# Kernel tuning notes

Measured on AMD Instinct MI355X. Metric: run time of the kernel, lower is better.

Reference implementation:

```python
import jax, jax.numpy as jnp
import numpy as np

N = 100000      # nodes
E = 1600000     # edges (avg degree 16)
D = 128         # in = hid = out dim


def setup_inputs() -> dict:
    key = jax.random.key(0)
    ks = jax.random.split(key, 7)
    x = jax.random.normal(ks[0], (N, D), dtype=jnp.float32)
    src = jax.random.randint(ks[1], (E,), 0, N, dtype=jnp.int32)
    dst = jax.random.randint(ks[2], (E,), 0, N, dtype=jnp.int32)
    s = 1.0 / np.sqrt(2 * D)  # torch Linear default init bound
    W0 = jax.random.uniform(ks[3], (D, 2 * D), jnp.float32, -s, s)
    b0 = jax.random.uniform(ks[4], (D,), jnp.float32, -s, s)
    W1 = jax.random.uniform(ks[5], (D, 2 * D), jnp.float32, -s, s)
    b1 = jax.random.uniform(ks[6], (D,), jnp.float32, -s, s)
    return {"x": x, "src": src, "dst": dst, "W0": W0, "b0": b0, "W1": W1, "b1": b1}


def graph_conv_left(x, src, dst):
    """DGL GraphConv(norm='left', weight=False, bias=False):
    h_v = sum_{(u->v) in E} x_u / max(outdeg(u), 1)."""
    n = x.shape[0]
    deg = jax.ops.segment_sum(jnp.ones_like(src, dtype=x.dtype), src, num_segments=n)
    deg = jnp.maximum(deg, 1.0)
    msgs = (x / deg[:, None])[src]          # [E, D] gather of normalized src feats
    return jax.ops.segment_sum(msgs, dst, num_segments=n)  # [N, D] scatter-add


def reference(x, src, dst, W0, b0, W1, b1):
    # layer 0: concat(self, agg) -> linear -> relu
    h = jnp.concatenate([x, graph_conv_left(x, src, dst)], axis=1)  # [N, 2D]
    h = jax.nn.relu(h @ W0.T + b0)                                  # [N, D]
    # layer 1 (output): concat -> linear (no relu)
    out = jnp.concatenate([h, graph_conv_left(h, src, dst)], axis=1) @ W1.T + b1
    return out
```

## Files before the change

### kernel.cpp

```cpp
#include <hip/hip_runtime.h>
#include <hip/hip_fp16.h>

#define DIM 128
#define CAP 64
#define BW_LOG 9
#define BW_NODES 512
#define MAXNB 256
#define SCAP 10240
#define CHUNK_P 2048
#define WSTRIDE 264

typedef _Float16 f16x8 __attribute__((ext_vector_type(8)));
typedef float f32x4 __attribute__((ext_vector_type(4)));
typedef unsigned int uint;

__global__ __launch_bounds__(256) void k_prep(const float* __restrict__ W0,
                                              const float* __restrict__ W1,
                                              const float* __restrict__ x,
                                              __half* __restrict__ Wh0,
                                              __half* __restrict__ Wh1,
                                              __half* __restrict__ fh,
                                              uint* __restrict__ curD,
                                              uint* __restrict__ curS,
                                              int NB, int nquadX) {
    int i = blockIdx.x * 256 + threadIdx.x;
    if (i < NB) { curD[i] = (uint)i * SCAP; curS[i] = (uint)i * SCAP; }
    const float* in; __half* out; int q;
    if (i < 8192)        { in = W0; out = Wh0; q = i; }
    else if (i < 16384)  { in = W1; out = Wh1; q = i - 8192; }
    else {
        q = i - 16384;
        if (q >= nquadX) return;
        in = x; out = fh;
    }
    float4 v = ((const float4*)in)[q];
    __half2* o = (__half2*)out;
    o[q * 2]     = __floats2half2_rn(v.x, v.y);
    o[q * 2 + 1] = __floats2half2_rn(v.z, v.w);
}

__global__ __launch_bounds__(256) void k_scatter(const int* __restrict__ src,
                                                 const int* __restrict__ dst,
                                                 uint* __restrict__ curD,
                                                 uint* __restrict__ curS,
                                                 uint* __restrict__ dbuf,
                                                 uint* __restrict__ sbuf,
                                                 int E, int NB, int nchunk) {
    __shared__ uint cb[MAXNB], bb[MAXNB], rb[MAXNB];
    for (int i = threadIdx.x; i < NB; i += 256) { cb[i] = 0; rb[i] = 0; }
    __syncthreads();
    bool isD = (int)blockIdx.x < nchunk;
    int chunk = isD ? blockIdx.x : blockIdx.x - nchunk;
    int e0 = chunk * CHUNK_P;
    int e1 = min(e0 + CHUNK_P, E);

    int4 sv[2], dv[2];
    bool ok[2];
    uint* cur  = isD ? curD : curS;
    uint* obuf = isD ? dbuf : sbuf;

#pragma unroll
    for (int q = 0; q < 2; ++q) {
        int i4 = (e0 >> 2) + q * 256 + (int)threadIdx.x;
        int e = i4 << 2;
        ok[q] = (e < e1);
        if (ok[q]) {
            sv[q] = ((const int4*)src)[i4];
            if (isD) dv[q] = ((const int4*)dst)[i4];
            int4 key = isD ? dv[q] : sv[q];
            atomicAdd(&cb[key.x >> BW_LOG], 1);
            atomicAdd(&cb[key.y >> BW_LOG], 1);
            atomicAdd(&cb[key.z >> BW_LOG], 1);
            atomicAdd(&cb[key.w >> BW_LOG], 1);
        }
    }
    __syncthreads();
    for (int i = threadIdx.x; i < NB; i += 256)
        if (cb[i]) bb[i] = atomicAdd(&cur[i], cb[i]);
    __syncthreads();
#pragma unroll
    for (int q = 0; q < 2; ++q) {
        if (!ok[q]) continue;
        int ks[4] = {isD ? dv[q].x : sv[q].x, isD ? dv[q].y : sv[q].y,
                     isD ? dv[q].z : sv[q].z, isD ? dv[q].w : sv[q].w};
        int ps[4] = {sv[q].x, sv[q].y, sv[q].z, sv[q].w};
#pragma unroll
        for (int k = 0; k < 4; ++k) {
            uint bkt = (uint)ks[k] >> BW_LOG;
            uint r = atomicAdd(&rb[bkt], 1);
            uint pos = bb[bkt] + r;
            uint pay = isD ? (((uint)(ks[k] & (BW_NODES - 1)) << 17) | (uint)ps[k])
                           : (uint)ps[k];
            if (pos < (bkt + 1) * SCAP) obuf[pos] = pay;
        }
    }
}

__global__ __launch_bounds__(256) void k_build_both(const uint* __restrict__ dbuf,
                                                    const uint* __restrict__ curD,
                                                    int* __restrict__ edge_pad,
                                                    int* __restrict__ cnt,
                                                    const uint* __restrict__ sbuf,
                                                    const uint* __restrict__ curS,
                                                    float* __restrict__ invd,
                                                    int N, int NB) {
    __shared__ uint cur[BW_NODES];
    for (int i = threadIdx.x; i < BW_NODES; i += 256) cur[i] = 0;
    __syncthreads();
    if ((int)blockIdx.x < NB) {
        int b = blockIdx.x;
        uint base = (uint)b * SCAP;
        uint total = curD[b] - base;
        if (total > SCAP) total = SCAP;
        int node0 = b << BW_LOG;
        for (uint i = threadIdx.x; i < total; i += 256) {
            uint v = dbuf[base + i];
            uint local = v >> 17;
            uint s = v & 0x1FFFFu;
            uint slot = atomicAdd(&cur[local], 1);
            if (slot < CAP)
                edge_pad[(size_t)(node0 + (int)local) * CAP + slot] = (int)s;
        }
        __syncthreads();
        for (int i = threadIdx.x; i < BW_NODES; i += 256) {
            int node = node0 + i;
            if (node < N) cnt[node] = (int)(cur[i] < CAP ? cur[i] : CAP);
        }
    } else {
        int b = blockIdx.x - NB;
        uint base = (uint)b * SCAP;
        uint total = curS[b] - base;
        if (total > SCAP) total = SCAP;
        int node0 = b << BW_LOG;
        for (uint i = threadIdx.x; i < total; i += 256)
            atomicAdd(&cur[sbuf[base + i] & (BW_NODES - 1)], 1);
        __syncthreads();
        for (int i = threadIdx.x; i < BW_NODES; i += 256) {
            int node = node0 + i;
            if (node < N) {
                uint d = cur[i];
                invd[node] = 1.0f / (float)(d > 1 ? d : 1);
            }
        }
    }
}

__global__ __launch_bounds__(256) void k_gather(const __half* __restrict__ feat,
                                                const float* __restrict__ invd,
                                                const int* __restrict__ edge_pad,
                                                const int* __restrict__ cnt_arr,
                                                __half* __restrict__ agg, int n) {
    int v = blockIdx.x * 4 + (threadIdx.x >> 6);
    int lane = threadIdx.x & 63;
    int quad = lane >> 4;
    int lq   = lane & 15;
    if (v >= n) return;
    int cnt = cnt_arr[v];
    if (cnt > CAP) cnt = CAP;

    int u_lane = 0;
    float w_lane = 0.f;
    if (lane < cnt) {
        u_lane = edge_pad[(size_t)v * CAP + lane];
        w_lane = invd[u_lane];
    }

    float acc[8] = {0.f, 0.f, 0.f, 0.f, 0.f, 0.f, 0.f, 0.f};
    int cntUp = (cnt + 7) & ~7;
    for (int j = 0; j < cntUp; j += 8) {
        int   ua = __shfl(u_lane, j + quad);
        float wa = __shfl(w_lane, j + quad);
        int   ub = __shfl(u_lane, j + 4 + quad);
        float wb = __shfl(w_lane, j + 4 + quad);
        uint4 ra = *(const uint4*)&feat[(size_t)ua * 128 + lq * 8];
        uint4 rb = *(const uint4*)&feat[(size_t)ub * 128 + lq * 8];
        const __half2* pa = (const __half2*)&ra;
        const __half2* pb = (const __half2*)&rb;
#pragma unroll
        for (int i = 0; i < 4; ++i) {
            float2 fa = __half22float2(pa[i]);
            float2 fb = __half22float2(pb[i]);
            acc[2 * i]     = fmaf(fa.x, wa, acc[2 * i]);
            acc[2 * i + 1] = fmaf(fa.y, wa, acc[2 * i + 1]);
            acc[2 * i]     = fmaf(fb.x, wb, acc[2 * i]);
            acc[2 * i + 1] = fmaf(fb.y, wb, acc[2 * i + 1]);
        }
    }
#pragma unroll
    for (int off = 16; off <= 32; off <<= 1) {
#pragma unroll
        for (int i = 0; i < 8; ++i) acc[i] += __shfl_xor(acc[i], off);
    }
    if (quad == 0) {
        __half2 o[4];
#pragma unroll
        for (int i = 0; i < 4; ++i) o[i] = __floats2half2_rn(acc[2 * i], acc[2 * i + 1]);
        *(uint4*)&agg[(size_t)v * 128 + lq * 8] = *(const uint4*)o;
    }
}

template <bool RELU, bool OUT16>
__global__ __launch_bounds__(256) void k_gemm_f16(const _Float16* __restrict__ A0,
                                                  const _Float16* __restrict__ A1,
                                                  const _Float16* __restrict__ Wh,
                                                  const float* __restrict__ bias,
                                                  float* __restrict__ out32,
                                                  _Float16* __restrict__ out16,
                                                  int n_rows) {
    __shared__ _Float16 Ws[128 * WSTRIDE];
    int tid  = threadIdx.x;
    int wave = tid >> 6;
    int lane = tid & 63;
    int quad = lane >> 4;
    int l16  = lane & 15;
    int m0 = blockIdx.x * 128 + wave * 32;

#pragma unroll
    for (int i = 0; i < 16; ++i) {
        int chunk = i * 256 + tid;
        int r = chunk >> 5;
        int c = (chunk & 31) * 8;
        *(f16x8*)&Ws[r * WSTRIDE + c] = *(const f16x8*)&Wh[r * 256 + c];
    }
    __syncthreads();

    f32x4 acc[2][8] = {};

    int ra = m0 + l16;
    int rb = m0 + 16 + l16;
    size_t r0 = (size_t)(ra < n_rows ? ra : 0);
    size_t r1 = (size_t)(rb < n_rows ? rb : 0);

#pragma unroll
    for (int ks = 0; ks < 8; ++ks) {
        int k0 = ks * 32;
        const _Float16* Ab = (k0 < 128) ? A0 : A1;
        int kk = (k0 & 127) + quad * 8;
        f16x8 a0 = *(const f16x8*)&Ab[r0 * 128 + kk];
        f16x8 a1 = *(const f16x8*)&Ab[r1 * 128 + kk];
        f16x8 b[8];
#pragma unroll
        for (int t = 0; t < 8; ++t)
            b[t] = *(const f16x8*)&Ws[(t * 16 + l16) * WSTRIDE + k0 + quad * 8];
#pragma unroll
        for (int t = 0; t < 8; ++t) {
            acc[0][t] = __builtin_amdgcn_mfma_f32_16x16x32_f16(a0, b[t], acc[0][t], 0, 0, 0);
            acc[1][t] = __builtin_amdgcn_mfma_f32_16x16x32_f16(a1, b[t], acc[1][t], 0, 0, 0);
        }
    }

#pragma unroll
    for (int t = 0; t < 8; ++t) {
        int col = t * 16 + l16;
        float bv = bias[col];
#pragma unroll
        for (int g = 0; g < 2; ++g) {
#pragma unroll
            for (int r = 0; r < 4; ++r) {
                int row = m0 + g * 16 + quad * 4 + r;
                if (row < n_rows) {
                    float v = acc[g][t][r] + bv;
                    if (RELU) v = fmaxf(v, 0.f);
                    if (OUT16) out16[(size_t)row * 128 + col] = (_Float16)v;
                    else       out32[(size_t)row * 128 + col] = v;
                }
            }
        }
    }
}

extern "C" void kernel_launch(void* const* d_in, const int* in_sizes, int n_in,
                              void* d_out, int out_size, void* d_ws, size_t ws_size,
                              hipStream_t stream) {
    const float* x  = (const float*)d_in[0];
    const int*   src = (const int*)d_in[1];
    const int*   dst = (const int*)d_in[2];
    const float* W0 = (const float*)d_in[3];
    const float* b0 = (const float*)d_in[4];
    const float* W1 = (const float*)d_in[5];
    const float* b1 = (const float*)d_in[6];
    int N = in_sizes[0] / DIM;
    int E = in_sizes[1];
    float* out = (float*)d_out;
    int NB = (N + BW_NODES - 1) >> BW_LOG;

    char* p = (char*)d_ws;
    uint* curD = (uint*)p; p += MAXNB * 4;
    uint* curS = (uint*)p; p += MAXNB * 4;
    int*   edge_pad = (int*)p;   p += (size_t)N * CAP * 4;
    int*   cnt      = (int*)p;   p += (size_t)N * 4;
    float* invd     = (float*)p; p += (size_t)N * 4;
    char*  uni = p;
    size_t bufSz = (size_t)2 * NB * SCAP * 4;
    size_t uniSz = bufSz > (size_t)N * DIM * 2 ? bufSz : (size_t)N * DIM * 2;
    p += uniSz;
    uint*   dbuf = (uint*)uni;
    uint*   sbuf = (uint*)(uni + (size_t)NB * SCAP * 4);
    __half* aggh = (__half*)uni;
    __half* fh   = (__half*)p; p += (size_t)N * DIM * 2;
    __half* hh   = (__half*)p; p += (size_t)N * DIM * 2;
    __half* Wh0  = (__half*)p; p += 128 * 256 * 2;
    __half* Wh1  = (__half*)p; p += 128 * 256 * 2;
    (void)ws_size; (void)n_in; (void)out_size;

    int nquadX = N * DIM / 4;
    int gP = (16384 + nquadX + 255) / 256;
    k_prep<<<gP, 256, 0, stream>>>(W0, W1, x, Wh0, Wh1, fh, curD, curS, NB, nquadX);

    int nchunk = (E + CHUNK_P - 1) / CHUNK_P;
    k_scatter<<<2 * nchunk, 256, 0, stream>>>(src, dst, curD, curS, dbuf, sbuf,
                                              E, NB, nchunk);
    k_build_both<<<2 * NB, 256, 0, stream>>>(dbuf, curD, edge_pad, cnt,
                                             sbuf, curS, invd, N, NB);

    int gG = (N + 3) / 4;
    int gM = (N + 127) / 128;

    k_gather<<<gG, 256, 0, stream>>>(fh, invd, edge_pad, cnt, aggh, N);
    k_gemm_f16<true, true><<<gM, 256, 0, stream>>>((const _Float16*)fh, (const _Float16*)aggh,
                                                   (const _Float16*)Wh0, b0,
                                                   nullptr, (_Float16*)hh, N);

    k_gather<<<gG, 256, 0, stream>>>(hh, invd, edge_pad, cnt, aggh, N);
    k_gemm_f16<false, false><<<gM, 256, 0, stream>>>((const _Float16*)hh, (const _Float16*)aggh,
                                                     (const _Float16*)Wh1, b1,
                                                     out, nullptr, N);
}
```

Baseline: 357.2 us.

## Compute out-degree via global atomics instead of a second bucketed scatter pass

Source-degree counting no longer uses separate src-bucketed scatter blocks and build blocks. It is done with a global atomicAdd per edge into a zeroed deg array inside the dst scatter kernel. Per-bucket cursors are padded to separate cache lines to reduce atomic contention, and the build kernel now runs one 512-thread block per dst bucket and reads deg to form invd. This removes half the scatter and build work and the sbuf traffic, in exchange for 1.6M global atomics with random addresses.

Measured after the change: 389.9 us. 1.09x slower.

```diff
diff --git a/kernel.cpp b/kernel.cpp
--- a/kernel.cpp
+++ b/kernel.cpp
@@ -8,6 +8,7 @@
 #define MAXNB 256
 #define SCAP 10240
 #define CHUNK_P 2048
+#define CURSTRIDE 16
 #define WSTRIDE 264
 
 typedef _Float16 f16x8 __attribute__((ext_vector_type(8)));
@@ -21,10 +22,11 @@
                                               __half* __restrict__ Wh1,
                                               __half* __restrict__ fh,
                                               uint* __restrict__ curD,
-                                              uint* __restrict__ curS,
-                                              int NB, int nquadX) {
+                                              uint* __restrict__ deg,
+                                              int NB, int N, int nquadX) {
     int i = blockIdx.x * 256 + threadIdx.x;
-    if (i < NB) { curD[i] = (uint)i * SCAP; curS[i] = (uint)i * SCAP; }
+    if (i < NB) curD[i * CURSTRIDE] = (uint)i * SCAP;
+    if (i < N) deg[i] = 0u;
     const float* in; __half* out; int q;
     if (i < 8192)        { in = W0; out = Wh0; q = i; }
     else if (i < 16384)  { in = W1; out = Wh1; q = i - 8192; }
@@ -42,22 +44,17 @@
 __global__ __launch_bounds__(256) void k_scatter(const int* __restrict__ src,
                                                  const int* __restrict__ dst,
                                                  uint* __restrict__ curD,
-                                                 uint* __restrict__ curS,
+                                                 uint* __restrict__ deg,
                                                  uint* __restrict__ dbuf,
-                                                 uint* __restrict__ sbuf,
-                                                 int E, int NB, int nchunk) {
+                                                 int E, int NB) {
     __shared__ uint cb[MAXNB], bb[MAXNB], rb[MAXNB];
     for (int i = threadIdx.x; i < NB; i += 256) { cb[i] = 0; rb[i] = 0; }
     __syncthreads();
-    bool isD = (int)blockIdx.x < nchunk;
-    int chunk = isD ? blockIdx.x : blockIdx.x - nchunk;
-    int e0 = chunk * CHUNK_P;
+    int e0 = blockIdx.x * CHUNK_P;
     int e1 = min(e0 + CHUNK_P, E);
 
     int4 sv[2], dv[2];
     bool ok[2];
-    uint* cur  = isD ? curD : curS;
-    uint* obuf = isD ? dbuf : sbuf;
 
 #pragma unroll
     for (int q = 0; q < 2; ++q) {
@@ -66,81 +63,64 @@
         ok[q] = (e < e1);
         if (ok[q]) {
             sv[q] = ((const int4*)src)[i4];
-            if (isD) dv[q] = ((const int4*)dst)[i4];
-            int4 key = isD ? dv[q] : sv[q];
-            atomicAdd(&cb[key.x >> BW_LOG], 1);
-            atomicAdd(&cb[key.y >> BW_LOG], 1);
-            atomicAdd(&cb[key.z >> BW_LOG], 1);
-            atomicAdd(&cb[key.w >> BW_LOG], 1);
+            dv[q] = ((const int4*)dst)[i4];
+            atomicAdd(&cb[dv[q].x >> BW_LOG], 1);
+            atomicAdd(&cb[dv[q].y >> BW_LOG], 1);
+            atomicAdd(&cb[dv[q].z >> BW_LOG], 1);
+            atomicAdd(&cb[dv[q].w >> BW_LOG], 1);
         }
     }
     __syncthreads();
     for (int i = threadIdx.x; i < NB; i += 256)
-        if (cb[i]) bb[i] = atomicAdd(&cur[i], cb[i]);
+        if (cb[i]) bb[i] = atomicAdd(&curD[i * CURSTRIDE], cb[i]);
     __syncthreads();
 #pragma unroll
     for (int q = 0; q < 2; ++q) {
         if (!ok[q]) continue;
-        int ks[4] = {isD ? dv[q].x : sv[q].x, isD ? dv[q].y : sv[q].y,
-                     isD ? dv[q].z : sv[q].z, isD ? dv[q].w : sv[q].w};
+        int ks[4] = {dv[q].x, dv[q].y, dv[q].z, dv[q].w};
         int ps[4] = {sv[q].x, sv[q].y, sv[q].z, sv[q].w};
 #pragma unroll
         for (int k = 0; k < 4; ++k) {
+            atomicAdd(&deg[ps[k]], 1u);
             uint bkt = (uint)ks[k] >> BW_LOG;
             uint r = atomicAdd(&rb[bkt], 1);
             uint pos = bb[bkt] + r;
-            uint pay = isD ? (((uint)(ks[k] & (BW_NODES - 1)) << 17) | (uint)ps[k])
-                           : (uint)ps[k];
-            if (pos < (bkt + 1) * SCAP) obuf[pos] = pay;
-        }
-    }
-}
-
-__global__ __launch_bounds__(256) void k_build_both(const uint* __restrict__ dbuf,
-                                                    const uint* __restrict__ curD,
-                                                    int* __restrict__ edge_pad,
-                                                    int* __restrict__ cnt,
-                                                    const uint* __restrict__ sbuf,
-                                                    const uint* __restrict__ curS,
-                                                    float* __restrict__ invd,
-                                                    int N, int NB) {
+            uint pay = ((uint)(ks[k] & (BW_NODES - 1)) << 17) | (uint)ps[k];
+            if (pos < (bkt + 1) * SCAP) dbuf[pos] = pay;
+        }
+    }
+}
+
+__global__ __launch_bounds__(512) void k_build(const uint* __restrict__ dbuf,
+                                               const uint* __restrict__ curD,
+                                               const uint* __restrict__ deg,
+                                               int* __restrict__ edge_pad,
+                                               int* __restrict__ cnt,
+                                               float* __restrict__ invd,
+                                               int N) {
     __shared__ uint cur[BW_NODES];
-    for (int i = threadIdx.x; i < BW_NODES; i += 256) cur[i] = 0;
-    __syncthreads();
-    if ((int)blockIdx.x < NB) {
-        int b = blockIdx.x;
-        uint base = (uint)b * SCAP;
-        uint total = curD[b] - base;
-        if (total > SCAP) total = SCAP;
-        int node0 = b << BW_LOG;
-        for (uint i = threadIdx.x; i < total; i += 256) {
-            uint v = dbuf[base + i];
-            uint local = v >> 17;
-            uint s = v & 0x1FFFFu;
-            uint slot = atomicAdd(&cur[local], 1);
-            if (slot < CAP)
-                edge_pad[(size_t)(node0 + (int)local) * CAP + slot] = (int)s;
-        }
-        __syncthreads();
-        for (int i = threadIdx.x; i < BW_NODES; i += 256) {
-            int node = node0 + i;
-            if (node < N) cnt[node] = (int)(cur[i] < CAP ? cur[i] : CAP);
-        }
-    } else {
-        int b = blockIdx.x - NB;
-        uint base = (uint)b * SCAP;
-        uint total = curS[b] - base;
-        if (total > SCAP) total = SCAP;
-        int node0 = b << BW_LOG;
-        for (uint i = threadIdx.x; i < total; i += 256)
-            atomicAdd(&cur[sbuf[base + i] & (BW_NODES - 1)], 1);
-        __syncthreads();
-        for (int i = threadIdx.x; i < BW_NODES; i += 256) {
-            int node = node0 + i;
-            if (node < N) {
-                uint d = cur[i];
-                invd[node] = 1.0f / (float)(d > 1 ? d : 1);
-            }
+    for (int i = threadIdx.x; i < BW_NODES; i += 512) cur[i] = 0;
+    __syncthreads();
+    int b = blockIdx.x;
+    uint base = (uint)b * SCAP;
+    uint total = curD[b * CURSTRIDE] - base;
+    if (total > SCAP) total = SCAP;
+    int node0 = b << BW_LOG;
+    for (uint i = threadIdx.x; i < total; i += 512) {
+        uint v = dbuf[base + i];
+        uint local = v >> 17;
+        uint s = v & 0x1FFFFu;
+        uint slot = atomicAdd(&cur[local], 1);
+        if (slot < CAP)
+            edge_pad[(size_t)(node0 + (int)local) * CAP + slot] = (int)s;
+    }
+    __syncthreads();
+    for (int i = threadIdx.x; i < BW_NODES; i += 512) {
+        int node = node0 + i;
+        if (node < N) {
+            cnt[node] = (int)(cur[i] < CAP ? cur[i] : CAP);
+            uint d = deg[node];
+            invd[node] = 1.0f / (float)(d > 1u ? d : 1u);
         }
     }
 }
@@ -285,17 +265,16 @@
     int NB = (N + BW_NODES - 1) >> BW_LOG;
 
     char* p = (char*)d_ws;
-    uint* curD = (uint*)p; p += MAXNB * 4;
-    uint* curS = (uint*)p; p += MAXNB * 4;
+    uint* curD = (uint*)p; p += MAXNB * CURSTRIDE * 4;
+    uint* deg  = (uint*)p; p += (size_t)N * 4;
     int*   edge_pad = (int*)p;   p += (size_t)N * CAP * 4;
     int*   cnt      = (int*)p;   p += (size_t)N * 4;
     float* invd     = (float*)p; p += (size_t)N * 4;
     char*  uni = p;
-    size_t bufSz = (size_t)2 * NB * SCAP * 4;
+    size_t bufSz = (size_t)NB * SCAP * 4;
     size_t uniSz = bufSz > (size_t)N * DIM * 2 ? bufSz : (size_t)N * DIM * 2;
     p += uniSz;
     uint*   dbuf = (uint*)uni;
-    uint*   sbuf = (uint*)(uni + (size_t)NB * SCAP * 4);
     __half* aggh = (__half*)uni;
     __half* fh   = (__half*)p; p += (size_t)N * DIM * 2;
     __half* hh   = (__half*)p; p += (size_t)N * DIM * 2;
@@ -305,13 +284,11 @@
 
     int nquadX = N * DIM / 4;
     int gP = (16384 + nquadX + 255) / 256;
-    k_prep<<<gP, 256, 0, stream>>>(W0, W1, x, Wh0, Wh1, fh, curD, curS, NB, nquadX);
+    k_prep<<<gP, 256, 0, stream>>>(W0, W1, x, Wh0, Wh1, fh, curD, deg, NB, N, nquadX);
 
     int nchunk = (E + CHUNK_P - 1) / CHUNK_P;
-    k_scatter<<<2 * nchunk, 256, 0, stream>>>(src, dst, curD, curS, dbuf, sbuf,
-                                              E, NB, nchunk);
-    k_build_both<<<2 * NB, 256, 0, stream>>>(dbuf, curD, edge_pad, cnt,
-                                             sbuf, curS, invd, N, NB);
+    k_scatter<<<nchunk, 256, 0, stream>>>(src, dst, curD, deg, dbuf, E, NB);
+    k_build<<<NB, 512, 0, stream>>>(dbuf, curD, deg, edge_pad, cnt, invd, N);
 
     int gG = (N + 3) / 4;
     int gM = (N + 127) / 128;
```
